# Optimization experiments

Measured on AMD Instinct MI355X. Metric: run time of the kernel, lower is better.

## Reference

```python
import jax, jax.numpy as jnp
import numpy as np

T = 65536   # total tokens across all packed sequences
C = 768     # channels
K = 5       # kernel_size (odd)
NSEQ = 16   # number of packed sequences (>1 -> masked varlen path)


def setup_inputs() -> dict:
    key = jax.random.key(0)
    k1, k2, k3, k4 = jax.random.split(key, 4)
    x = jax.random.normal(k1, (T, C), dtype=jnp.float32)
    # cu_seqlens: [0, sorted interior boundaries, T]
    interior = jnp.sort(jax.random.randint(k2, (NSEQ - 1,), 1, T)).astype(jnp.int32)
    cu_seqlens = jnp.concatenate([
        jnp.zeros((1,), dtype=jnp.int32),
        interior,
        jnp.full((1,), T, dtype=jnp.int32),
    ])
    # depthwise conv weight [C, K] (== conv.weight[:, 0, :]) and bias [C]
    weight = jax.random.normal(k3, (C, K), dtype=jnp.float32) * 0.1
    bias = jax.random.normal(k4, (C,), dtype=jnp.float32) * 0.01
    return {"x": x, "cu_seqlens": cu_seqlens, "weight": weight, "bias": bias}


def reference(x, cu_seqlens, weight, bias):
    # Varlen Canon depthwise mixing with sequence-boundary masking.
    # x: [T, C] float32; cu_seqlens: [n_seqs+1] int32; weight: [C, K]; bias: [C].
    t = x.shape[0]
    radius = weight.shape[1] // 2
    positions = jnp.arange(t, dtype=cu_seqlens.dtype)
    # seq_id[i] = which packed sequence token i belongs to
    seq_id = jnp.searchsorted(cu_seqlens[1:], positions, side='right')
    out = jnp.zeros_like(x)
    for k, offset in enumerate(range(-radius, radius + 1)):  # K taps (small fixed loop)
        rolled_x = jnp.roll(x, -offset, axis=0)
        rolled_id = jnp.roll(seq_id, -offset, axis=0)
        valid = (rolled_id == seq_id)[:, None]               # [T, 1] boundary mask
        out = out + jnp.where(valid, rolled_x, 0.0) * weight[:, k]
    out = out + bias
    return x + out  # residual add
```

## Files before the change

### kernel.cpp

```cpp
#include <hip/hip_runtime.h>


#define CC  768
#define C4V (CC / 4)
#define KK  5
#define RR  2
#define TPB 16

__global__ __launch_bounds__(C4V) void canon_dwconv_kernel(
    const float4* __restrict__ x4,
    const int*    __restrict__ cu,
    int nseq,
    const float*  __restrict__ weight,
    const float4* __restrict__ bias4,
    float4*       __restrict__ out4,
    int T)
{
    const int c4 = threadIdx.x;
    const int t0 = (int)blockIdx.x * TPB;
    const int c  = c4 * 4;

    float w[KK][4];
#pragma unroll
    for (int j = 0; j < 4; ++j)
#pragma unroll
        for (int k = 0; k < KK; ++k)
            w[k][j] = weight[(c + j) * KK + k];

    const float4 b = bias4[c4];

    float4 win[KK];
#pragma unroll
    for (int i = 0; i < KK - 1; ++i) {
        int r  = t0 - RR + i;
        int rc = min(max(r, 0), T - 1);
        win[i] = x4[(size_t)rc * C4V + c4];
    }

    int sid = 0;
    while (sid < nseq && cu[sid + 1] <= t0) ++sid;

#pragma unroll
    for (int tt = 0; tt < TPB; ++tt) {
        const int t = t0 + tt;
        if (t < T) {
            {
                int rc = min(t + RR, T - 1);
                win[(tt + KK - 1) % KK] = x4[(size_t)rc * C4V + c4];
            }
            while (sid < nseq && cu[sid + 1] <= t) ++sid;
            const int start = cu[sid];
            const int end   = cu[sid + 1];

            const float4 r0 = win[(tt + 0) % KK];
            const float4 r1 = win[(tt + 1) % KK];
            const float4 r2 = win[(tt + 2) % KK];
            const float4 r3 = win[(tt + 3) % KK];
            const float4 r4 = win[(tt + 4) % KK];

            const float m0 = (t - 2 >= start) ? 1.0f : 0.0f;
            const float m1 = (t - 1 >= start) ? 1.0f : 0.0f;
            const float m3 = (t + 1 <  end)  ? 1.0f : 0.0f;
            const float m4 = (t + 2 <  end)  ? 1.0f : 0.0f;

            float4 o;
            o.x = r2.x + b.x + r2.x * w[2][0]
                + r0.x * (w[0][0] * m0) + r1.x * (w[1][0] * m1)
                + r3.x * (w[3][0] * m3) + r4.x * (w[4][0] * m4);
            o.y = r2.y + b.y + r2.y * w[2][1]
                + r0.y * (w[0][1] * m0) + r1.y * (w[1][1] * m1)
                + r3.y * (w[3][1] * m3) + r4.y * (w[4][1] * m4);
            o.z = r2.z + b.z + r2.z * w[2][2]
                + r0.z * (w[0][2] * m0) + r1.z * (w[1][2] * m1)
                + r3.z * (w[3][2] * m3) + r4.z * (w[4][2] * m4);
            o.w = r2.w + b.w + r2.w * w[2][3]
                + r0.w * (w[0][3] * m0) + r1.w * (w[1][3] * m1)
                + r3.w * (w[3][3] * m3) + r4.w * (w[4][3] * m4);

            out4[(size_t)t * C4V + c4] = o;
        }
    }
}

extern "C" void kernel_launch(void* const* d_in, const int* in_sizes, int n_in,
                              void* d_out, int out_size, void* d_ws, size_t ws_size,
                              hipStream_t stream) {
    const float4* x4     = (const float4*)d_in[0];
    const int*    cu     = (const int*)d_in[1];
    const float*  weight = (const float*)d_in[2];
    const float4* bias4  = (const float4*)d_in[3];
    float4*       out4   = (float4*)d_out;

    const int T    = in_sizes[0] / CC;
    const int nseq = in_sizes[1] - 1;

    const int grid = (T + TPB - 1) / TPB;
    canon_dwconv_kernel<<<grid, C4V, 0, stream>>>(x4, cu, nseq, weight, bias4, out4, T);
}
```

Before: 347.5 us.

## Add boundary-free fast path, nontemporal stores, vector weight loads, larger token tile

Blocks whose whole token range plus halo lies inside one sequence now take a fast path with no masks, no clamping and no per-token search through cu_seqlens. Other blocks keep the masked path. Output writes use nontemporal stores to avoid polluting the cache, weights are read as float4, and each block now covers 32 tokens instead of 16 with an occupancy hint. The larger tile halves the grid and may reduce parallelism. The kernel is memory-bound, so the overall effect is likely limited.

```diff
diff --git a/kernel.cpp b/kernel.cpp
--- a/kernel.cpp
+++ b/kernel.cpp
@@ -5,52 +5,56 @@
 #define C4V (CC / 4)
 #define KK  5
 #define RR  2
-#define TPB 16
+#define TPB 32
 
-__global__ __launch_bounds__(C4V) void canon_dwconv_kernel(
+typedef float nfloat4 __attribute__((ext_vector_type(4)));
+
+__device__ __forceinline__ void nt_store(float4* p, const float4& v) {
+    __builtin_nontemporal_store(*reinterpret_cast<const nfloat4*>(&v),
+                                reinterpret_cast<nfloat4*>(p));
+}
+
+#define W(k, j) wl[(j) * KK + (k)]
+
+__global__ __launch_bounds__(C4V, 4) void canon_dwconv_kernel(
     const float4* __restrict__ x4,
     const int*    __restrict__ cu,
     int nseq,
-    const float*  __restrict__ weight,
+    const float4* __restrict__ w4,
     const float4* __restrict__ bias4,
     float4*       __restrict__ out4,
     int T)
 {
     const int c4 = threadIdx.x;
     const int t0 = (int)blockIdx.x * TPB;
-    const int c  = c4 * 4;
 
-    float w[KK][4];
+    float wl[KK * 4];
 #pragma unroll
-    for (int j = 0; j < 4; ++j)
-#pragma unroll
-        for (int k = 0; k < KK; ++k)
-            w[k][j] = weight[(c + j) * KK + k];
-
+    for (int i = 0; i < KK; ++i) {
+        const float4 v = w4[c4 * KK + i];
+        wl[4 * i + 0] = v.x; wl[4 * i + 1] = v.y;
+        wl[4 * i + 2] = v.z; wl[4 * i + 3] = v.w;
+    }
     const float4 b = bias4[c4];
-
-    float4 win[KK];
-#pragma unroll
-    for (int i = 0; i < KK - 1; ++i) {
-        int r  = t0 - RR + i;
-        int rc = min(max(r, 0), T - 1);
-        win[i] = x4[(size_t)rc * C4V + c4];
-    }
 
     int sid = 0;
     while (sid < nseq && cu[sid + 1] <= t0) ++sid;
+    const int s0 = cu[sid];
+    const int e0 = cu[sid + 1];
+
+    const float4* __restrict__ xrow = x4 + c4;
+    float4*       __restrict__ orow = out4 + c4;
+
+    if (s0 <= t0 - RR && e0 >= t0 + TPB + RR) {
+        float4 win[KK];
+#pragma unroll
+        for (int i = 0; i < KK - 1; ++i)
+            win[i] = xrow[(size_t)(t0 - RR + i) * C4V];
 
 #pragma unroll
-    for (int tt = 0; tt < TPB; ++tt) {
-        const int t = t0 + tt;
-        if (t < T) {
-            {
-                int rc = min(t + RR, T - 1);
-                win[(tt + KK - 1) % KK] = x4[(size_t)rc * C4V + c4];
-            }
-            while (sid < nseq && cu[sid + 1] <= t) ++sid;
-            const int start = cu[sid];
-            const int end   = cu[sid + 1];
+        for (int tt = 0; tt < TPB; ++tt) {
+            const int t = t0 + tt;
+            win[(tt + KK - 1) % KK] = xrow[(size_t)(t + RR) * C4V];
 
             const float4 r0 = win[(tt + 0) % KK];
             const float4 r1 = win[(tt + 1) % KK];
@@ -58,26 +62,69 @@
             const float4 r3 = win[(tt + 3) % KK];
             const float4 r4 = win[(tt + 4) % KK];
 
-            const float m0 = (t - 2 >= start) ? 1.0f : 0.0f;
-            const float m1 = (t - 1 >= start) ? 1.0f : 0.0f;
-            const float m3 = (t + 1 <  end)  ? 1.0f : 0.0f;
-            const float m4 = (t + 2 <  end)  ? 1.0f : 0.0f;
+            float4 o;
+            o.x = r2.x + b.x + r2.x * W(2,0)
+                + r0.x * W(0,0) + r1.x * W(1,0)
+                + r3.x * W(3,0) + r4.x * W(4,0);
+            o.y = r2.y + b.y + r2.y * W(2,1)
+                + r0.y * W(0,1) + r1.y * W(1,1)
+                + r3.y * W(3,1) + r4.y * W(4,1);
+            o.z = r2.z + b.z + r2.z * W(2,2)
+                + r0.z * W(0,2) + r1.z * W(1,2)
+                + r3.z * W(3,2) + r4.z * W(4,2);
+            o.w = r2.w + b.w + r2.w * W(2,3)
+                + r0.w * W(0,3) + r1.w * W(1,3)
+                + r3.w * W(3,3) + r4.w * W(4,3);
 
-            float4 o;
-            o.x = r2.x + b.x + r2.x * w[2][0]
-                + r0.x * (w[0][0] * m0) + r1.x * (w[1][0] * m1)
-                + r3.x * (w[3][0] * m3) + r4.x * (w[4][0] * m4);
-            o.y = r2.y + b.y + r2.y * w[2][1]
-                + r0.y * (w[0][1] * m0) + r1.y * (w[1][1] * m1)
-                + r3.y * (w[3][1] * m3) + r4.y * (w[4][1] * m4);
-            o.z = r2.z + b.z + r2.z * w[2][2]
-                + r0.z * (w[0][2] * m0) + r1.z * (w[1][2] * m1)
-                + r3.z * (w[3][2] * m3) + r4.z * (w[4][2] * m4);
-            o.w = r2.w + b.w + r2.w * w[2][3]
-                + r0.w * (w[0][3] * m0) + r1.w * (w[1][3] * m1)
-                + r3.w * (w[3][3] * m3) + r4.w * (w[4][3] * m4);
+            nt_store(&orow[(size_t)t * C4V], o);
+        }
+    } else {
+        float4 win[KK];
+#pragma unroll
+        for (int i = 0; i < KK - 1; ++i) {
+            int r  = t0 - RR + i;
+            int rc = min(max(r, 0), T - 1);
+            win[i] = xrow[(size_t)rc * C4V];
+        }
 
-            out4[(size_t)t * C4V + c4] = o;
+#pragma unroll
+        for (int tt = 0; tt < TPB; ++tt) {
+            const int t = t0 + tt;
+            if (t < T) {
+                int rc = min(t + RR, T - 1);
+                win[(tt + KK - 1) % KK] = xrow[(size_t)rc * C4V];
+
+                while (sid < nseq && cu[sid + 1] <= t) ++sid;
+                const int start = cu[sid];
+                const int end   = cu[sid + 1];
+
+                const float4 r0 = win[(tt + 0) % KK];
+                const float4 r1 = win[(tt + 1) % KK];
+                const float4 r2 = win[(tt + 2) % KK];
+                const float4 r3 = win[(tt + 3) % KK];
+                const float4 r4 = win[(tt + 4) % KK];
+
+                const float m0 = (t - 2 >= start) ? 1.0f : 0.0f;
+                const float m1 = (t - 1 >= start) ? 1.0f : 0.0f;
+                const float m3 = (t + 1 <  end)  ? 1.0f : 0.0f;
+                const float m4 = (t + 2 <  end)  ? 1.0f : 0.0f;
+
+                float4 o;
+                o.x = r2.x + b.x + r2.x * W(2,0)
+                    + r0.x * (W(0,0) * m0) + r1.x * (W(1,0) * m1)
+                    + r3.x * (W(3,0) * m3) + r4.x * (W(4,0) * m4);
+                o.y = r2.y + b.y + r2.y * W(2,1)
+                    + r0.y * (W(0,1) * m0) + r1.y * (W(1,1) * m1)
+                    + r3.y * (W(3,1) * m3) + r4.y * (W(4,1) * m4);
+                o.z = r2.z + b.z + r2.z * W(2,2)
+                    + r0.z * (W(0,2) * m0) + r1.z * (W(1,2) * m1)
+                    + r3.z * (W(3,2) * m3) + r4.z * (W(4,2) * m4);
+                o.w = r2.w + b.w + r2.w * W(2,3)
+                    + r0.w * (W(0,3) * m0) + r1.w * (W(1,3) * m1)
+                    + r3.w * (W(3,3) * m3) + r4.w * (W(4,3) * m4);
+
+                nt_store(&orow[(size_t)t * C4V], o);
+            }
         }
     }
 }
@@ -87,7 +134,7 @@
                               hipStream_t stream) {
     const float4* x4     = (const float4*)d_in[0];
     const int*    cu     = (const int*)d_in[1];
-    const float*  weight = (const float*)d_in[2];
+    const float4* w4     = (const float4*)d_in[2];
     const float4* bias4  = (const float4*)d_in[3];
     float4*       out4   = (float4*)d_out;
 
@@ -95,5 +142,5 @@
     const int nseq = in_sizes[1] - 1;
 
     const int grid = (T + TPB - 1) / TPB;
-    canon_dwconv_kernel<<<grid, C4V, 0, stream>>>(x4, cu, nseq, weight, bias4, out4, T);
+    canon_dwconv_kernel<<<grid, C4V, 0, stream>>>(x4, cu, nseq, w4, bias4, out4, T);
 }
```

New measurement: 354.5 us. 1.02x slower.
